# Kernel optimization log

Hardware: AMD Instinct MI355X
Metric: run time of the kernel (lower is better)

Reference implementation:

```python
import jax, jax.numpy as jnp
import numpy as np

EPS = 1e-5

def _sage_conv(x, src, dst, Wl, bl, Wr, num_nodes):
    # PyG SAGEConv (mean aggr): out = lin_l(mean_{j->i} x_j) + lin_r(x_i)
    msg = x[src]                                              # [E, F]
    s = jax.ops.segment_sum(msg, dst, num_segments=num_nodes) # [N, F]
    deg = jax.ops.segment_sum(jnp.ones(src.shape, x.dtype), dst, num_segments=num_nodes)
    mean = s / jnp.maximum(deg, 1.0)[:, None]
    return mean @ Wl + bl + x @ Wr

def _bn(x, gamma, beta):
    # BatchNorm1d in training mode: biased batch statistics
    m = x.mean(axis=0)
    v = x.var(axis=0)
    return (x - m) * jax.lax.rsqrt(v + EPS) * gamma + beta

def setup_inputs() -> dict:
    key = jax.random.key(0)
    ks = jax.random.split(key, 16)
    N, F, H, H1, H2 = 50000, 100, 128, 128, 64
    E = 800000
    def xav(k, fan_in, fan_out):
        lim = float(np.sqrt(6.0 / (fan_in + fan_out)))
        return jax.random.uniform(k, (fan_in, fan_out), jnp.float32, -lim, lim)
    return {
        "x": jax.random.normal(ks[0], (N, F), jnp.float32),
        "edge_index": jax.random.randint(ks[1], (2, E), 0, N, jnp.int32),
        "Wl1": xav(ks[2], F, H), "bl1": jnp.zeros((H,), jnp.float32), "Wr1": xav(ks[3], F, H),
        "Wl2": xav(ks[4], H, H), "bl2": jnp.zeros((H,), jnp.float32), "Wr2": xav(ks[5], H, H),
        "W1": xav(ks[6], H, H1), "b1": jnp.zeros((H1,), jnp.float32),
        "g1": jnp.ones((H1,), jnp.float32), "be1": jnp.zeros((H1,), jnp.float32),
        "W2": xav(ks[7], H1, H2), "b2": jnp.zeros((H2,), jnp.float32),
        "g2": jnp.ones((H2,), jnp.float32), "be2": jnp.zeros((H2,), jnp.float32),
        "W3": xav(ks[8], H2, 1), "b3": jnp.zeros((1,), jnp.float32),
    }

def reference(x, edge_index, Wl1, bl1, Wr1, Wl2, bl2, Wr2,
              W1, b1, g1, be1, W2, b2, g2, be2, W3, b3):
    N = x.shape[0]
    src, dst = edge_index[0], edge_index[1]
    h1 = jax.nn.relu(_sage_conv(x, src, dst, Wl1, bl1, Wr1, N))   # [N, H]
    h2 = jax.nn.relu(_sage_conv(h1, src, dst, Wl2, bl2, Wr2, N))  # [N, H]
    z = jax.nn.relu(_bn(h2 @ W1 + b1, g1, be1))                   # [N, H1]
    z = jax.nn.relu(_bn(z @ W2 + b2, g2, be2))                    # [N, H2]
    out = (z @ W3 + b3).squeeze(-1)                               # [N]
    return out, h1, h2
```

## Files before the change

kernel.cpp:

```cpp
#include <hip/hip_runtime.h>

#define BN_EPS 1e-5f

typedef short s8v __attribute__((ext_vector_type(8)));
typedef float f4v __attribute__((ext_vector_type(4)));
typedef unsigned short u4v __attribute__((ext_vector_type(4)));

__device__ __forceinline__ unsigned short f2bf(float f) {
  union { float f; unsigned u; } v; v.f = f;
  unsigned r = v.u + 0x7FFF + ((v.u >> 16) & 1);
  return (unsigned short)(r >> 16);
}
__device__ __forceinline__ float bf2f(unsigned short u) {
  union { unsigned u; float f; } v; v.u = ((unsigned)u) << 16; return v.f;
}

__global__ __launch_bounds__(256) void deg_kernel(const int* __restrict__ dst,
                                                  int* __restrict__ deg, int E) {
  int e = blockIdx.x * 256 + threadIdx.x;
  if (e < E) atomicAdd(&deg[dst[e]], 1);
}

__global__ __launch_bounds__(256) void scan_partial_kernel(const int* __restrict__ deg,
    int* __restrict__ partials, int N) {
  __shared__ int sh[256];
  int t = threadIdx.x;
  int base = blockIdx.x * 1024 + t * 4;
  int s = 0;
#pragma unroll
  for (int i = 0; i < 4; ++i) {
    int idx = base + i;
    if (idx < N) s += deg[idx];
  }
  sh[t] = s;
  __syncthreads();
  for (int d = 128; d > 0; d >>= 1) {
    if (t < d) sh[t] += sh[t + d];
    __syncthreads();
  }
  if (t == 0) partials[blockIdx.x] = sh[0];
}

__global__ __launch_bounds__(256) void scan_offsets_kernel(const int* __restrict__ partials,
    int* __restrict__ blk_off, int G) {
  __shared__ int sh[256];
  int t = threadIdx.x;
  sh[t] = (t < G) ? partials[t] : 0;
  __syncthreads();
  for (int d = 1; d < 256; d <<= 1) {
    int v = (t >= d) ? sh[t - d] : 0;
    __syncthreads();
    sh[t] += v;
    __syncthreads();
  }
  if (t < G) blk_off[t] = (t == 0) ? 0 : sh[t - 1];
}

__global__ __launch_bounds__(256) void scan_scatter_kernel(const int* __restrict__ deg,
    const int* __restrict__ blk_off, int* __restrict__ row_start,
    int* __restrict__ gcursor, int N) {
  __shared__ int sh[256];
  int t = threadIdx.x;
  int base = blockIdx.x * 1024 + t * 4;
  int v[4];
#pragma unroll
  for (int i = 0; i < 4; ++i) v[i] = (base + i < N) ? deg[base + i] : 0;
  sh[t] = v[0] + v[1] + v[2] + v[3];
  __syncthreads();
  for (int d = 1; d < 256; d <<= 1) {
    int u = (t >= d) ? sh[t - d] : 0;
    __syncthreads();
    sh[t] += u;
    __syncthreads();
  }
  int off = blk_off[blockIdx.x] + ((t == 0) ? 0 : sh[t - 1]);
#pragma unroll
  for (int i = 0; i < 4; ++i) {
    int idx = base + i;
    if (idx < N) {
      row_start[idx] = off;
      if ((idx & 127) == 0) gcursor[idx >> 7] = off;
      off += v[i];
    }
  }
}

#define CHUNK 8192
#define NBMAX 512
__global__ __launch_bounds__(256) void csr_bucket_kernel(
    const int* __restrict__ src, const int* __restrict__ dst,
    int* __restrict__ gcursor, unsigned* __restrict__ pairs, int E) {
  __shared__ int h[NBMAX];
  __shared__ int off[NBMAX];
  __shared__ int cnt2[NBMAX];
  __shared__ int gadj[NBMAX];
  __shared__ unsigned pbuf[CHUNK];
  __shared__ unsigned short bidx[CHUNK];
  int t = threadIdx.x;
  int base = blockIdx.x * CHUNK;
  int cnt = min(CHUNK, E - base);
  for (int i = t; i < NBMAX; i += 256) { h[i] = 0; cnt2[i] = 0; }
  __syncthreads();
  for (int i = t; i < cnt; i += 256) atomicAdd(&h[dst[base + i] >> 7], 1);
  __syncthreads();
  off[t] = h[t]; off[t + 256] = h[t + 256];
  __syncthreads();
  for (int d = 1; d < 512; d <<= 1) {
    int v0 = (t >= d) ? off[t - d] : 0;
    int v1 = off[t + 256 - d];
    __syncthreads();
    off[t] += v0; off[t + 256] += v1;
    __syncthreads();
  }
  int e0 = off[t] - h[t];
  int e1 = off[t + 256] - h[t + 256];
  __syncthreads();
  off[t] = e0; off[t + 256] = e1;
  __syncthreads();
  for (int i = t; i < NBMAX; i += 256) {
    int c = h[i];
    if (c > 0) gadj[i] = atomicAdd(&gcursor[i], c) - off[i];
  }
  __syncthreads();
  for (int i = t; i < cnt; i += 256) {
    int s = src[base + i];
    int d = dst[base + i];
    int b = d >> 7;
    int p = off[b] + atomicAdd(&cnt2[b], 1);
    pbuf[p] = (unsigned)s | ((unsigned)d << 16);
    bidx[p] = (unsigned short)b;
  }
  __syncthreads();
  for (int i = t; i < cnt; i += 256)
    pairs[gadj[bidx[i]] + i] = pbuf[i];
}

__global__ __launch_bounds__(256) void csr_fill_kernel(
    const unsigned* __restrict__ pairs, const int* __restrict__ row_start,
    int* __restrict__ eidx, int N, int E) {
  __shared__ int cur[128];
  int b = blockIdx.x;
  int node0 = b << 7;
  int t = threadIdx.x;
  if (t < 128) {
    int node = node0 + t;
    cur[t] = (node < N) ? row_start[node] : 0;
  }
  __syncthreads();
  int pbeg = row_start[node0];
  int pend = (node0 + 128 < N) ? row_start[node0 + 128] : E;
  for (int i = pbeg + t; i < pend; i += 256) {
    unsigned p = pairs[i];
    int pos = atomicAdd(&cur[(int)(p >> 16) - node0], 1);
    eidx[pos] = (int)(p & 0xFFFFu);
  }
}

__global__ __launch_bounds__(256) void prep_kernel(
    const float* __restrict__ x, unsigned short* __restrict__ xb,
    const float* __restrict__ Wl1, const float* __restrict__ Wr1,
    const float* __restrict__ Wl2, const float* __restrict__ Wr2,
    const float* __restrict__ W1, const float* __restrict__ W2,
    unsigned short* __restrict__ Wl1t, unsigned short* __restrict__ Wr1t,
    unsigned short* __restrict__ Wl2t, unsigned short* __restrict__ Wr2t,
    unsigned short* __restrict__ W1t, unsigned short* __restrict__ W2t,
    int N, int xblocks) {
  int blk = blockIdx.x;
  if (blk < xblocks) {
    int t = blk * 256 + threadIdx.x;
    if (t < N * 128) {
      int col = t & 127;
      int n = t >> 7;
      xb[t] = (col < 100) ? f2bf(x[n * 100 + col]) : (unsigned short)0;
    }
    return;
  }
  int w = blk - xblocks;
  const float* W; unsigned short* Wt; int K, C, base;
  if (w < 64)       { W = Wl1; Wt = Wl1t; K = 100; C = 128; base = 0;   }
  else if (w < 128) { W = Wr1; Wt = Wr1t; K = 100; C = 128; base = 64;  }
  else if (w < 192) { W = Wl2; Wt = Wl2t; K = 128; C = 128; base = 128; }
  else if (w < 256) { W = Wr2; Wt = Wr2t; K = 128; C = 128; base = 192; }
  else if (w < 320) { W = W1;  Wt = W1t;  K = 128; C = 128; base = 256; }
  else              { W = W2;  Wt = W2t;  K = 128; C = 64;  base = 320; }
  int t = (w - base) * 256 + threadIdx.x;
  if (t >= C * 128) return;
  int c = t >> 7;
  int k = t & 127;
  Wt[t] = (k < K) ? f2bf(W[k * C + c]) : (unsigned short)0;
}

__global__ __launch_bounds__(256) void gather_kernel(
    const unsigned short* __restrict__ feat, const int* __restrict__ eidx,
    const int* __restrict__ row_start, const int* __restrict__ deg,
    unsigned short* __restrict__ mean_out, int N) {
  int wave = threadIdx.x >> 6;
  int lane = threadIdx.x & 63;
  int node = blockIdx.x * 4 + wave;
  if (node >= N) return;
  int beg = row_start[node];
  int d = deg[node];
  float a0 = 0.0f, a1 = 0.0f;
  for (int i0 = 0; i0 < d; i0 += 64) {
    int cnt = min(64, d - i0);
    int my = (lane < cnt) ? eidx[beg + i0 + lane] : 0;
    int j = 0;
    for (; j + 7 < cnt; j += 8) {
      int s0 = __shfl(my, j + 0);
      int s1 = __shfl(my, j + 1);
      int s2 = __shfl(my, j + 2);
      int s3 = __shfl(my, j + 3);
      int s4 = __shfl(my, j + 4);
      int s5 = __shfl(my, j + 5);
      int s6 = __shfl(my, j + 6);
      int s7 = __shfl(my, j + 7);
      unsigned v0 = ((const unsigned*)(feat + (size_t)s0 * 128))[lane];
      unsigned v1 = ((const unsigned*)(feat + (size_t)s1 * 128))[lane];
      unsigned v2 = ((const unsigned*)(feat + (size_t)s2 * 128))[lane];
      unsigned v3 = ((const unsigned*)(feat + (size_t)s3 * 128))[lane];
      unsigned v4 = ((const unsigned*)(feat + (size_t)s4 * 128))[lane];
      unsigned v5 = ((const unsigned*)(feat + (size_t)s5 * 128))[lane];
      unsigned v6 = ((const unsigned*)(feat + (size_t)s6 * 128))[lane];
      unsigned v7 = ((const unsigned*)(feat + (size_t)s7 * 128))[lane];
      a0 += bf2f((unsigned short)v0) + bf2f((unsigned short)v1)
          + bf2f((unsigned short)v2) + bf2f((unsigned short)v3)
          + bf2f((unsigned short)v4) + bf2f((unsigned short)v5)
          + bf2f((unsigned short)v6) + bf2f((unsigned short)v7);
      a1 += bf2f((unsigned short)(v0 >> 16)) + bf2f((unsigned short)(v1 >> 16))
          + bf2f((unsigned short)(v2 >> 16)) + bf2f((unsigned short)(v3 >> 16))
          + bf2f((unsigned short)(v4 >> 16)) + bf2f((unsigned short)(v5 >> 16))
          + bf2f((unsigned short)(v6 >> 16)) + bf2f((unsigned short)(v7 >> 16));
    }
    for (; j < cnt; ++j) {
      int s0 = __shfl(my, j);
      unsigned v0 = ((const unsigned*)(feat + (size_t)s0 * 128))[lane];
      a0 += bf2f((unsigned short)v0);
      a1 += bf2f((unsigned short)(v0 >> 16));
    }
  }
  float inv = 1.0f / fmaxf((float)d, 1.0f);
  unsigned o = (unsigned)f2bf(a0 * inv) | ((unsigned)f2bf(a1 * inv) << 16);
  ((unsigned*)(mean_out + (size_t)node * 128))[lane] = o;
}

__global__ __launch_bounds__(128) void bn_prep_kernel(const float* __restrict__ sum,
    const float* __restrict__ sq, const float* __restrict__ g,
    const float* __restrict__ be, float* __restrict__ bnp, int N) {
  int c = threadIdx.x;
  float S = 0.0f, SS = 0.0f;
#pragma unroll
  for (int k = 0; k < 8; ++k) { S += sum[k * 128 + c]; SS += sq[k * 128 + c]; }
  float invN = 1.0f / (float)N;
  float mn = S * invN;
  float var = SS * invN - mn * mn;
  float sc = g[c] * rsqrtf(var + BN_EPS);
  bnp[2 * c] = sc;
  bnp[2 * c + 1] = be[c] - mn * sc;
}

template<int COLS, bool DUAL, bool RELU, bool F32OUT, bool BF16OUT, bool STATS, bool BNIN>
__global__ __launch_bounds__(256, 4) void mfma_gemm_kernel(
    const unsigned short* __restrict__ A1, const unsigned short* __restrict__ W1t,
    const unsigned short* __restrict__ A2, const unsigned short* __restrict__ W2t,
    const float* __restrict__ bias, const float* __restrict__ bnp,
    float* __restrict__ outF, unsigned short* __restrict__ outB,
    float* __restrict__ sum, float* __restrict__ sq, int N) {
  constexpr int CTW = COLS / 64;
  constexpr int CH = COLS / 4;
  constexpr int RS = COLS + 4;
  constexpr int NA = DUAL ? 2 : 1;
  constexpr int OUT_OFF = 8192 * NA;
  constexpr int BNL_OFF = OUT_OFF + 32 * RS * 4;
  constexpr int SMEM_SZ = BNL_OFF + (BNIN ? 1024 : 0);
  __shared__ char smem[SMEM_SZ];
  float* outl = (float*)(smem + OUT_OFF);
  float* reds = (float*)smem;
  float* redq = (float*)(smem + 4096);
  float* bnl  = (float*)(smem + BNL_OFF);
  int t = threadIdx.x;
  int wave = t >> 6;
  int lane = t & 63;
  int quad = lane >> 4;
  int m = lane & 15;
  int blk = blockIdx.x * 32;
  int col0 = wave * (16 * CTW);

  if (BNIN) bnl[t] = bnp[t];

  s8v B1r[4][CTW], B2r[4][CTW];
  {
    int c0 = wave * 2, c1 = c0 + 1;
    const char* g1 = (const char*)A1 + (size_t)blk * 256;
    s8v va = *(const s8v*)(g1 + c0 * 1024 + lane * 16);
    s8v vb = *(const s8v*)(g1 + c1 * 1024 + lane * 16);
    s8v vc, vd;
    if (DUAL) {
      const char* g2 = (const char*)A2 + (size_t)blk * 256;
      vc = *(const s8v*)(g2 + c0 * 1024 + lane * 16);
      vd = *(const s8v*)(g2 + c1 * 1024 + lane * 16);
    }
#pragma unroll
    for (int kk = 0; kk < 4; ++kk)
#pragma unroll
      for (int ct = 0; ct < CTW; ++ct) {
        size_t wr = (size_t)(col0 + ct * 16 + m) * 128 + kk * 32 + quad * 8;
        B1r[kk][ct] = *(const s8v*)(W1t + wr);
        if (DUAL) B2r[kk][ct] = *(const s8v*)(W2t + wr);
      }
    int r0 = c0 * 4 + (lane >> 4);
    int r1 = r0 + 4;
    int cb = (lane & 15) << 4;
    *(s8v*)(smem + r0 * 256 + (cb ^ ((r0 & 7) << 4))) = va;
    *(s8v*)(smem + r1 * 256 + (cb ^ ((r1 & 7) << 4))) = vb;
    if (DUAL) {
      *(s8v*)(smem + 8192 + r0 * 256 + (cb ^ ((r0 & 7) << 4))) = vc;
      *(s8v*)(smem + 8192 + r1 * 256 + (cb ^ ((r1 & 7) << 4))) = vd;
    }
  }
  __syncthreads();

  f4v acc[2][CTW];
#pragma unroll
  for (int rf = 0; rf < 2; ++rf)
#pragma unroll
    for (int ct = 0; ct < CTW; ++ct) acc[rf][ct] = (f4v){0.f, 0.f, 0.f, 0.f};
#pragma unroll
  for (int kk = 0; kk < 4; ++kk) {
    int cb2 = kk * 64 + quad * 16;
    s8v a1[2], a2[2];
#pragma unroll
    for (int rf = 0; rf < 2; ++rf) {
      int rr = rf * 16 + m;
      int sw = rr * 256 + (cb2 ^ ((rr & 7) << 4));
      a1[rf] = *(const s8v*)(smem + sw);
      if (DUAL) a2[rf] = *(const s8v*)(smem + 8192 + sw);
    }
    if (BNIN) {
      float sc[8], sh[8];
#pragma unroll
      for (int i = 0; i < 8; ++i) {
        int c = kk * 32 + quad * 8 + i;
        sc[i] = bnl[2 * c]; sh[i] = bnl[2 * c + 1];
      }
#pragma unroll
      for (int rf = 0; rf < 2; ++rf) {
        s8v raw = a1[rf];
        s8v a;
#pragma unroll
        for (int i = 0; i < 8; ++i) {
          float v = bf2f((unsigned short)raw[i]);
          v = fmaxf(v * sc[i] + sh[i], 0.0f);
          a[i] = (short)f2bf(v);
        }
        a1[rf] = a;
      }
    }
#pragma unroll
    for (int ct = 0; ct < CTW; ++ct)
#pragma unroll
      for (int rf = 0; rf < 2; ++rf) {
        acc[rf][ct] = __builtin_amdgcn_mfma_f32_16x16x32_bf16(a1[rf], B1r[kk][ct], acc[rf][ct], 0, 0, 0);
        if (DUAL)
          acc[rf][ct] = __builtin_amdgcn_mfma_f32_16x16x32_bf16(a2[rf], B2r[kk][ct], acc[rf][ct], 0, 0, 0);
      }
  }

#pragma unroll
  for (int ct = 0; ct < CTW; ++ct) {
    int col = col0 + ct * 16 + m;
    float b = bias[col];
#pragma unroll
    for (int rf = 0; rf < 2; ++rf)
#pragma unroll
      for (int r = 0; r < 4; ++r) {
        float v = acc[rf][ct][r] + b;
        if (RELU) v = fmaxf(v, 0.0f);
        outl[(rf * 16 + quad * 4 + r) * RS + col] = v;
      }
  }
  __syncthreads();
  float s4[4] = {0.f, 0.f, 0.f, 0.f}, q4[4] = {0.f, 0.f, 0.f, 0.f};
  for (int idx = t; idx < 32 * CH; idx += 256) {
    int row = idx / CH;
    int c4 = idx % CH;
    int gr = blk + row;
    if (gr < N) {
      f4v v = *(const f4v*)&outl[row * RS + c4 * 4];
      if (F32OUT) *(f4v*)(outF + (size_t)gr * COLS + c4 * 4) = v;
      if (BF16OUT) {
        u4v o;
#pragma unroll
        for (int j = 0; j < 4; ++j) o[j] = f2bf(v[j]);
        *(u4v*)(outB + (size_t)gr * COLS + c4 * 4) = o;
      }
      if (STATS) {
#pragma unroll
        for (int j = 0; j < 4; ++j) { s4[j] += v[j]; q4[j] += v[j] * v[j]; }
      }
    }
  }
  if (STATS) {
    __syncthreads();
#pragma unroll
    for (int j = 0; j < 4; ++j) { reds[t * 4 + j] = s4[j]; redq[t * 4 + j] = q4[j]; }
    __syncthreads();
    if (t < COLS) {
      int c4 = t >> 2, j = t & 3;
      float S = 0.0f, SS = 0.0f;
#pragma unroll
      for (int g = 0; g < 256 / CH; ++g) {
        S  += reds[(g * CH + c4) * 4 + j];
        SS += redq[(g * CH + c4) * 4 + j];
      }
      int slot = (blockIdx.x & 7) * COLS + t;
      atomicAdd(&sum[slot], S);
      atomicAdd(&sq[slot], SS);
    }
  }
}

__global__ __launch_bounds__(256, 4) void sage_mlp_kernel(
    const unsigned short* __restrict__ A1,
    const unsigned short* __restrict__ Wlt,
    const unsigned short* __restrict__ A2,
    const unsigned short* __restrict__ Wrt,
    const float* __restrict__ bl,
    const unsigned short* __restrict__ W1t, const float* __restrict__ b1,
    float* __restrict__ h2out, unsigned short* __restrict__ y1b,
    float* __restrict__ sum, float* __restrict__ sq, int N) {
  constexpr int RS = 132;
  constexpr int OUT_OFF = 16384;
  __shared__ char smem[OUT_OFF + 32 * RS * 4];
  float* outl = (float*)(smem + OUT_OFF);
  float* reds = (float*)smem;
  float* redq = (float*)(smem + 4096);
  int t = threadIdx.x;
  int wave = t >> 6, lane = t & 63;
  int quad = lane >> 4, m = lane & 15;
  int blk = blockIdx.x * 32;
  int col0 = wave * 32;

  s8v BLr[4][2], BRr[4][2];
  {
    int c0 = wave * 2, c1 = c0 + 1;
    const char* g1 = (const char*)A1 + (size_t)blk * 256;
    const char* g2 = (const char*)A2 + (size_t)blk * 256;
    s8v va = *(const s8v*)(g1 + c0 * 1024 + lane * 16);
    s8v vb = *(const s8v*)(g1 + c1 * 1024 + lane * 16);
    s8v vc = *(const s8v*)(g2 + c0 * 1024 + lane * 16);
    s8v vd = *(const s8v*)(g2 + c1 * 1024 + lane * 16);
#pragma unroll
    for (int kk = 0; kk < 4; ++kk)
#pragma unroll
      for (int ct = 0; ct < 2; ++ct) {
        size_t wr = (size_t)(col0 + ct * 16 + m) * 128 + kk * 32 + quad * 8;
        BLr[kk][ct] = *(const s8v*)(Wlt + wr);
        BRr[kk][ct] = *(const s8v*)(Wrt + wr);
      }
    int r0 = c0 * 4 + (lane >> 4);
    int r1 = r0 + 4;
    int cb = (lane & 15) << 4;
    *(s8v*)(smem + r0 * 256 + (cb ^ ((r0 & 7) << 4))) = va;
    *(s8v*)(smem + r1 * 256 + (cb ^ ((r1 & 7) << 4))) = vb;
    *(s8v*)(smem + 8192 + r0 * 256 + (cb ^ ((r0 & 7) << 4))) = vc;
    *(s8v*)(smem + 8192 + r1 * 256 + (cb ^ ((r1 & 7) << 4))) = vd;
  }
  __syncthreads();

  f4v acc[2][2];
#pragma unroll
  for (int rf = 0; rf < 2; ++rf)
#pragma unroll
    for (int ct = 0; ct < 2; ++ct) acc[rf][ct] = (f4v){0.f, 0.f, 0.f, 0.f};
#pragma unroll
  for (int kk = 0; kk < 4; ++kk) {
    int cb2 = kk * 64 + quad * 16;
    s8v a1[2], a2[2];
#pragma unroll
    for (int rf = 0; rf < 2; ++rf) {
      int rr = rf * 16 + m;
      int sw = rr * 256 + (cb2 ^ ((rr & 7) << 4));
      a1[rf] = *(const s8v*)(smem + sw);
      a2[rf] = *(const s8v*)(smem + 8192 + sw);
    }
#pragma unroll
    for (int ct = 0; ct < 2; ++ct)
#pragma unroll
      for (int rf = 0; rf < 2; ++rf) {
        acc[rf][ct] = __builtin_amdgcn_mfma_f32_16x16x32_bf16(a1[rf], BLr[kk][ct], acc[rf][ct], 0, 0, 0);
        acc[rf][ct] = __builtin_amdgcn_mfma_f32_16x16x32_bf16(a2[rf], BRr[kk][ct], acc[rf][ct], 0, 0, 0);
      }
  }

  s8v bw[4][2];
#pragma unroll
  for (int kk = 0; kk < 4; ++kk)
#pragma unroll
    for (int ct = 0; ct < 2; ++ct)
      bw[kk][ct] = *(const s8v*)(W1t + (size_t)(col0 + ct * 16 + m) * 128 + kk * 32 + quad * 8);

#pragma unroll
  for (int ct = 0; ct < 2; ++ct) {
    int col = col0 + ct * 16 + m;
    float b = bl[col];
#pragma unroll
    for (int rf = 0; rf < 2; ++rf)
#pragma unroll
      for (int r = 0; r < 4; ++r)
        outl[(rf * 16 + quad * 4 + r) * RS + col] = fmaxf(acc[rf][ct][r] + b, 0.0f);
  }
  __syncthreads();

  for (int idx = t; idx < 32 * 32; idx += 256) {
    int row = idx >> 5;
    int c4 = idx & 31;
    int gr = blk + row;
    if (gr < N)
      *(f4v*)(h2out + (size_t)gr * 128 + c4 * 4) = *(const f4v*)&outl[row * RS + c4 * 4];
  }

  s8v af[2][4];
#pragma unroll
  for (int rf = 0; rf < 2; ++rf)
#pragma unroll
    for (int kk = 0; kk < 4; ++kk) {
      int k0 = kk * 32 + quad * 8;
      f4v x0 = *(const f4v*)&outl[(rf * 16 + m) * RS + k0];
      f4v x1 = *(const f4v*)&outl[(rf * 16 + m) * RS + k0 + 4];
      s8v a;
#pragma unroll
      for (int i = 0; i < 4; ++i) { a[i] = (short)f2bf(x0[i]); a[4 + i] = (short)f2bf(x1[i]); }
      af[rf][kk] = a;
    }

  f4v acc2[2][2];
#pragma unroll
  for (int rf = 0; rf < 2; ++rf)
#pragma unroll
    for (int ct = 0; ct < 2; ++ct) acc2[rf][ct] = (f4v){0.f, 0.f, 0.f, 0.f};
#pragma unroll
  for (int kk = 0; kk < 4; ++kk)
#pragma unroll
    for (int ct = 0; ct < 2; ++ct)
#pragma unroll
      for (int rf = 0; rf < 2; ++rf)
        acc2[rf][ct] = __builtin_amdgcn_mfma_f32_16x16x32_bf16(af[rf][kk], bw[kk][ct], acc2[rf][ct], 0, 0, 0);
  __syncthreads();
#pragma unroll
  for (int ct = 0; ct < 2; ++ct) {
    int col = col0 + ct * 16 + m;
    float b = b1[col];
#pragma unroll
    for (int rf = 0; rf < 2; ++rf)
#pragma unroll
      for (int r = 0; r < 4; ++r)
        outl[(rf * 16 + quad * 4 + r) * RS + col] = acc2[rf][ct][r] + b;
  }
  __syncthreads();

  float s4[4] = {0.f, 0.f, 0.f, 0.f}, q4[4] = {0.f, 0.f, 0.f, 0.f};
  for (int idx = t; idx < 32 * 32; idx += 256) {
    int row = idx >> 5;
    int c4 = idx & 31;
    int gr = blk + row;
    if (gr < N) {
      f4v v = *(const f4v*)&outl[row * RS + c4 * 4];
      u4v o;
#pragma unroll
      for (int j = 0; j < 4; ++j) o[j] = f2bf(v[j]);
      *(u4v*)(y1b + (size_t)gr * 128 + c4 * 4) = o;
#pragma unroll
      for (int j = 0; j < 4; ++j) { s4[j] += v[j]; q4[j] += v[j] * v[j]; }
    }
  }
#pragma unroll
  for (int j = 0; j < 4; ++j) { reds[t * 4 + j] = s4[j]; redq[t * 4 + j] = q4[j]; }
  __syncthreads();
  if (t < 128) {
    int c4 = t >> 2, j = t & 3;
    float S = 0.0f, SS = 0.0f;
#pragma unroll
    for (int g = 0; g < 8; ++g) {
      S  += reds[(g * 32 + c4) * 4 + j];
      SS += redq[(g * 32 + c4) * 4 + j];
    }
    int slot = (blockIdx.x & 7) * 128 + t;
    atomicAdd(&sum[slot], S);
    atomicAdd(&sq[slot], SS);
  }
}

__global__ __launch_bounds__(256) void bn_head_kernel(const float* __restrict__ y2,
    const float* __restrict__ sum, const float* __restrict__ sumsq,
    const float* __restrict__ g, const float* __restrict__ be,
    const float* __restrict__ W3, const float* __restrict__ b3,
    float* __restrict__ out, int N) {
  int wave = threadIdx.x >> 6;
  int lane = threadIdx.x & 63;
  int row = blockIdx.x * 4 + wave;
  if (row >= N) return;
  float S = 0.0f, SS = 0.0f;
#pragma unroll
  for (int k = 0; k < 8; ++k) { S += sum[k * 64 + lane]; SS += sumsq[k * 64 + lane]; }
  float invN = 1.0f / (float)N;
  float m = S * invN;
  float var = SS * invN - m * m;
  float val = (y2[(size_t)row * 64 + lane] - m) * rsqrtf(var + BN_EPS) * g[lane] + be[lane];
  val = fmaxf(val, 0.0f) * W3[lane];
#pragma unroll
  for (int off = 32; off > 0; off >>= 1) val += __shfl_down(val, off);
  if (lane == 0) out[row] = val + b3[0];
}

extern "C" void kernel_launch(void* const* d_in, const int* in_sizes, int n_in,
                              void* d_out, int out_size, void* d_ws, size_t ws_size,
                              hipStream_t stream) {
  const int F = 100, H = 128;
  const int N = in_sizes[0] / F;
  const int E = in_sizes[1] / 2;

  const float* x   = (const float*)d_in[0];
  const int* edge  = (const int*)d_in[1];
  const int* src   = edge;
  const int* dst   = edge + E;
  const float* Wl1 = (const float*)d_in[2];
  const float* bl1 = (const float*)d_in[3];
  const float* Wr1 = (const float*)d_in[4];
  const float* Wl2 = (const float*)d_in[5];
  const float* bl2 = (const float*)d_in[6];
  const float* Wr2 = (const float*)d_in[7];
  const float* W1  = (const float*)d_in[8];
  const float* b1  = (const float*)d_in[9];
  const float* g1  = (const float*)d_in[10];
  const float* be1 = (const float*)d_in[11];
  const float* W2  = (const float*)d_in[12];
  const float* b2  = (const float*)d_in[13];
  const float* g2  = (const float*)d_in[14];
  const float* be2 = (const float*)d_in[15];
  const float* W3  = (const float*)d_in[16];
  const float* b3  = (const float*)d_in[17];

  float* out0 = (float*)d_out;
  float* h1   = out0 + N;
  float* h2   = h1 + (size_t)N * H;

  const int SCAN_G = (N + 1023) / 1024;
  const int NB = (N + 127) / 128;

  char* wsp = (char*)d_ws;
  int* deg       = (int*)wsp;               wsp += (size_t)N * sizeof(int);
  int* row_start = (int*)wsp;               wsp += (size_t)N * sizeof(int);
  int* eidx      = (int*)wsp;               wsp += (size_t)E * sizeof(int);
  unsigned* pairs = (unsigned*)wsp;         wsp += (size_t)E * sizeof(unsigned);
  int* gcursor   = (int*)wsp;               wsp += 512 * sizeof(int);
  int* partials  = (int*)wsp;               wsp += 256 * sizeof(int);
  int* blk_off   = (int*)wsp;               wsp += 256 * sizeof(int);
  float* sum1    = (float*)wsp;             wsp += 8 * 128 * sizeof(float);
  float* sq1     = (float*)wsp;             wsp += 8 * 128 * sizeof(float);
  float* sum2    = (float*)wsp;             wsp += 8 * 64 * sizeof(float);
  float* sq2     = (float*)wsp;             wsp += 8 * 64 * sizeof(float);
  float* bnp     = (float*)wsp;             wsp += 256 * sizeof(float);
  float* bufA    = (float*)wsp;             wsp += (size_t)N * 128 * sizeof(float);
  unsigned short* bfX = (unsigned short*)wsp; wsp += (size_t)N * 128 * 2;
  unsigned short* bfM = (unsigned short*)wsp; wsp += (size_t)N * 128 * 2;
  unsigned short* bfH = (unsigned short*)wsp; wsp += (size_t)N * 128 * 2;
  unsigned short* Wl1t = (unsigned short*)wsp; wsp += 128 * 128 * 2;
  unsigned short* Wr1t = (unsigned short*)wsp; wsp += 128 * 128 * 2;
  unsigned short* Wl2t = (unsigned short*)wsp; wsp += 128 * 128 * 2;
  unsigned short* Wr2t = (unsigned short*)wsp; wsp += 128 * 128 * 2;
  unsigned short* W1t  = (unsigned short*)wsp; wsp += 128 * 128 * 2;
  unsigned short* W2t  = (unsigned short*)wsp; wsp += 64 * 128 * 2;

  unsigned short* y1b = (unsigned short*)bufA;
  float* y2 = (float*)((char*)bufA + (size_t)N * 128 * 2);

  hipMemsetAsync(deg, 0, (size_t)N * sizeof(int), stream);
  hipMemsetAsync(sum1, 0, (8 * 128 + 8 * 128 + 8 * 64 + 8 * 64) * sizeof(float), stream);

  deg_kernel<<<(E + 255) / 256, 256, 0, stream>>>(dst, deg, E);
  scan_partial_kernel<<<SCAN_G, 256, 0, stream>>>(deg, partials, N);
  scan_offsets_kernel<<<1, 256, 0, stream>>>(partials, blk_off, SCAN_G);
  scan_scatter_kernel<<<SCAN_G, 256, 0, stream>>>(deg, blk_off, row_start, gcursor, N);
  csr_bucket_kernel<<<(E + CHUNK - 1) / CHUNK, 256, 0, stream>>>(src, dst, gcursor, pairs, E);
  csr_fill_kernel<<<NB, 256, 0, stream>>>(pairs, row_start, eidx, N, E);

  int xblocks = ((size_t)N * 128 + 255) / 256;
  prep_kernel<<<xblocks + 352, 256, 0, stream>>>(x, bfX,
      Wl1, Wr1, Wl2, Wr2, W1, W2, Wl1t, Wr1t, Wl2t, Wr2t, W1t, W2t, N, xblocks);

  int gemm_grid = (N + 31) / 32;

  gather_kernel<<<(N + 3) / 4, 256, 0, stream>>>(bfX, eidx, row_start, deg, bfM, N);
  mfma_gemm_kernel<128, true, true, true, true, false, false><<<gemm_grid, 256, 0, stream>>>(
      bfM, Wl1t, bfX, Wr1t, bl1, nullptr, h1, bfH, nullptr, nullptr, N);

  gather_kernel<<<(N + 3) / 4, 256, 0, stream>>>(bfH, eidx, row_start, deg, bfM, N);
  sage_mlp_kernel<<<gemm_grid, 256, 0, stream>>>(
      bfM, Wl2t, bfH, Wr2t, bl2, W1t, b1, h2, y1b, sum1, sq1, N);

  bn_prep_kernel<<<1, 128, 0, stream>>>(sum1, sq1, g1, be1, bnp, N);

  mfma_gemm_kernel<64, false, false, true, false, true, true><<<gemm_grid, 256, 0, stream>>>(
      y1b, W2t, nullptr, nullptr, b2, bnp, y2, nullptr, sum2, sq2, N);

  bn_head_kernel<<<(N + 3) / 4, 256, 0, stream>>>(
      y2, sum2, sq2, g2, be2, W3, b3, out0, N);
}
```

Baseline: 323.5 us.

## Merge small setup kernels and fold BN prep into GEMM to cut launches

Folds the degree-count atomics into the prep kernel and replaces the three-kernel prefix scan with a single 1024-thread block scan. The BN statistics finalisation is now computed redundantly in each block of the second MLP GEMM, so bn_prep_kernel is gone, and the two memsets are merged into one by placing the BN accumulators next to the degree array. It also halves the CSR bucket chunk size and raises the occupancy hint for the non-dual GEMM. The intent is to remove several kernel launches and serialization points, at the cost of a serial single-block scan and repeated per-block BN math.

```diff
diff --git a/kernel.cpp b/kernel.cpp
--- a/kernel.cpp
+++ b/kernel.cpp
@@ -15,77 +15,78 @@
   union { unsigned u; float f; } v; v.u = ((unsigned)u) << 16; return v.f;
 }
 
-__global__ __launch_bounds__(256) void deg_kernel(const int* __restrict__ dst,
-                                                  int* __restrict__ deg, int E) {
-  int e = blockIdx.x * 256 + threadIdx.x;
-  if (e < E) atomicAdd(&deg[dst[e]], 1);
-}
-
-__global__ __launch_bounds__(256) void scan_partial_kernel(const int* __restrict__ deg,
-    int* __restrict__ partials, int N) {
-  __shared__ int sh[256];
+__global__ __launch_bounds__(256) void prep_kernel(
+    const int* __restrict__ dst, int* __restrict__ deg, int E, int degB,
+    const float* __restrict__ x, unsigned short* __restrict__ xb,
+    const float* __restrict__ Wl1, const float* __restrict__ Wr1,
+    const float* __restrict__ Wl2, const float* __restrict__ Wr2,
+    const float* __restrict__ W1, const float* __restrict__ W2,
+    unsigned short* __restrict__ Wl1t, unsigned short* __restrict__ Wr1t,
+    unsigned short* __restrict__ Wl2t, unsigned short* __restrict__ Wr2t,
+    unsigned short* __restrict__ W1t, unsigned short* __restrict__ W2t,
+    int N, int xblocks) {
+  int blk = blockIdx.x;
+  if (blk < degB) {
+    int e = blk * 256 + threadIdx.x;
+    if (e < E) atomicAdd(&deg[dst[e]], 1);
+    return;
+  }
+  blk -= degB;
+  if (blk < xblocks) {
+    int t = blk * 256 + threadIdx.x;
+    if (t < N * 128) {
+      int col = t & 127;
+      int n = t >> 7;
+      xb[t] = (col < 100) ? f2bf(x[n * 100 + col]) : (unsigned short)0;
+    }
+    return;
+  }
+  int w = blk - xblocks;
+  const float* W; unsigned short* Wt; int K, C, base;
+  if (w < 64)       { W = Wl1; Wt = Wl1t; K = 100; C = 128; base = 0;   }
+  else if (w < 128) { W = Wr1; Wt = Wr1t; K = 100; C = 128; base = 64;  }
+  else if (w < 192) { W = Wl2; Wt = Wl2t; K = 128; C = 128; base = 128; }
+  else if (w < 256) { W = Wr2; Wt = Wr2t; K = 128; C = 128; base = 192; }
+  else if (w < 320) { W = W1;  Wt = W1t;  K = 128; C = 128; base = 256; }
+  else              { W = W2;  Wt = W2t;  K = 128; C = 64;  base = 320; }
+  int t = (w - base) * 256 + threadIdx.x;
+  if (t >= C * 128) return;
+  int c = t >> 7;
+  int k = t & 127;
+  Wt[t] = (k < K) ? f2bf(W[k * C + c]) : (unsigned short)0;
+}
+
+__global__ __launch_bounds__(1024) void scan_all_kernel(const int* __restrict__ deg,
+    int* __restrict__ row_start, int* __restrict__ gcursor, int N) {
+  __shared__ int ws[1024];
   int t = threadIdx.x;
-  int base = blockIdx.x * 1024 + t * 4;
+  int PER = (N + 1023) >> 10;
+  int base = t * PER;
   int s = 0;
-#pragma unroll
-  for (int i = 0; i < 4; ++i) {
+  for (int i = 0; i < PER; ++i) {
     int idx = base + i;
     if (idx < N) s += deg[idx];
   }
-  sh[t] = s;
-  __syncthreads();
-  for (int d = 128; d > 0; d >>= 1) {
-    if (t < d) sh[t] += sh[t + d];
+  ws[t] = s;
+  __syncthreads();
+  for (int d = 1; d < 1024; d <<= 1) {
+    int v = (t >= d) ? ws[t - d] : 0;
     __syncthreads();
-  }
-  if (t == 0) partials[blockIdx.x] = sh[0];
-}
-
-__global__ __launch_bounds__(256) void scan_offsets_kernel(const int* __restrict__ partials,
-    int* __restrict__ blk_off, int G) {
-  __shared__ int sh[256];
-  int t = threadIdx.x;
-  sh[t] = (t < G) ? partials[t] : 0;
-  __syncthreads();
-  for (int d = 1; d < 256; d <<= 1) {
-    int v = (t >= d) ? sh[t - d] : 0;
+    ws[t] += v;
     __syncthreads();
-    sh[t] += v;
-    __syncthreads();
-  }
-  if (t < G) blk_off[t] = (t == 0) ? 0 : sh[t - 1];
-}
-
-__global__ __launch_bounds__(256) void scan_scatter_kernel(const int* __restrict__ deg,
-    const int* __restrict__ blk_off, int* __restrict__ row_start,
-    int* __restrict__ gcursor, int N) {
-  __shared__ int sh[256];
-  int t = threadIdx.x;
-  int base = blockIdx.x * 1024 + t * 4;
-  int v[4];
-#pragma unroll
-  for (int i = 0; i < 4; ++i) v[i] = (base + i < N) ? deg[base + i] : 0;
-  sh[t] = v[0] + v[1] + v[2] + v[3];
-  __syncthreads();
-  for (int d = 1; d < 256; d <<= 1) {
-    int u = (t >= d) ? sh[t - d] : 0;
-    __syncthreads();
-    sh[t] += u;
-    __syncthreads();
-  }
-  int off = blk_off[blockIdx.x] + ((t == 0) ? 0 : sh[t - 1]);
-#pragma unroll
-  for (int i = 0; i < 4; ++i) {
+  }
+  int off = (t == 0) ? 0 : ws[t - 1];
+  for (int i = 0; i < PER; ++i) {
     int idx = base + i;
     if (idx < N) {
       row_start[idx] = off;
       if ((idx & 127) == 0) gcursor[idx >> 7] = off;
-      off += v[i];
-    }
-  }
-}
-
-#define CHUNK 8192
+      off += deg[idx];
+    }
+  }
+}
+
+#define CHUNK 4096
 #define NBMAX 512
 __global__ __launch_bounds__(256) void csr_bucket_kernel(
     const int* __restrict__ src, const int* __restrict__ dst,
@@ -154,40 +155,6 @@
     int pos = atomicAdd(&cur[(int)(p >> 16) - node0], 1);
     eidx[pos] = (int)(p & 0xFFFFu);
   }
-}
-
-__global__ __launch_bounds__(256) void prep_kernel(
-    const float* __restrict__ x, unsigned short* __restrict__ xb,
-    const float* __restrict__ Wl1, const float* __restrict__ Wr1,
-    const float* __restrict__ Wl2, const float* __restrict__ Wr2,
-    const float* __restrict__ W1, const float* __restrict__ W2,
-    unsigned short* __restrict__ Wl1t, unsigned short* __restrict__ Wr1t,
-    unsigned short* __restrict__ Wl2t, unsigned short* __restrict__ Wr2t,
-    unsigned short* __restrict__ W1t, unsigned short* __restrict__ W2t,
-    int N, int xblocks) {
-  int blk = blockIdx.x;
-  if (blk < xblocks) {
-    int t = blk * 256 + threadIdx.x;
-    if (t < N * 128) {
-      int col = t & 127;
-      int n = t >> 7;
-      xb[t] = (col < 100) ? f2bf(x[n * 100 + col]) : (unsigned short)0;
-    }
-    return;
-  }
-  int w = blk - xblocks;
-  const float* W; unsigned short* Wt; int K, C, base;
-  if (w < 64)       { W = Wl1; Wt = Wl1t; K = 100; C = 128; base = 0;   }
-  else if (w < 128) { W = Wr1; Wt = Wr1t; K = 100; C = 128; base = 64;  }
-  else if (w < 192) { W = Wl2; Wt = Wl2t; K = 128; C = 128; base = 128; }
-  else if (w < 256) { W = Wr2; Wt = Wr2t; K = 128; C = 128; base = 192; }
-  else if (w < 320) { W = W1;  Wt = W1t;  K = 128; C = 128; base = 256; }
-  else              { W = W2;  Wt = W2t;  K = 128; C = 64;  base = 320; }
-  int t = (w - base) * 256 + threadIdx.x;
-  if (t >= C * 128) return;
-  int c = t >> 7;
-  int k = t & 127;
-  Wt[t] = (k < K) ? f2bf(W[k * C + c]) : (unsigned short)0;
 }
 
 __global__ __launch_bounds__(256) void gather_kernel(
@@ -243,26 +210,13 @@
   ((unsigned*)(mean_out + (size_t)node * 128))[lane] = o;
 }
 
-__global__ __launch_bounds__(128) void bn_prep_kernel(const float* __restrict__ sum,
-    const float* __restrict__ sq, const float* __restrict__ g,
-    const float* __restrict__ be, float* __restrict__ bnp, int N) {
-  int c = threadIdx.x;
-  float S = 0.0f, SS = 0.0f;
-#pragma unroll
-  for (int k = 0; k < 8; ++k) { S += sum[k * 128 + c]; SS += sq[k * 128 + c]; }
-  float invN = 1.0f / (float)N;
-  float mn = S * invN;
-  float var = SS * invN - mn * mn;
-  float sc = g[c] * rsqrtf(var + BN_EPS);
-  bnp[2 * c] = sc;
-  bnp[2 * c + 1] = be[c] - mn * sc;
-}
-
 template<int COLS, bool DUAL, bool RELU, bool F32OUT, bool BF16OUT, bool STATS, bool BNIN>
-__global__ __launch_bounds__(256, 4) void mfma_gemm_kernel(
+__global__ __launch_bounds__(256, DUAL ? 4 : 5) void mfma_gemm_kernel(
     const unsigned short* __restrict__ A1, const unsigned short* __restrict__ W1t,
     const unsigned short* __restrict__ A2, const unsigned short* __restrict__ W2t,
-    const float* __restrict__ bias, const float* __restrict__ bnp,
+    const float* __restrict__ bias,
+    const float* __restrict__ bsum, const float* __restrict__ bsq,
+    const float* __restrict__ bg, const float* __restrict__ bbe,
     float* __restrict__ outF, unsigned short* __restrict__ outB,
     float* __restrict__ sum, float* __restrict__ sq, int N) {
   constexpr int CTW = COLS / 64;
@@ -285,7 +239,17 @@
   int blk = blockIdx.x * 32;
   int col0 = wave * (16 * CTW);
 
-  if (BNIN) bnl[t] = bnp[t];
+  if (BNIN && t < 128) {
+    float S = 0.0f, SS = 0.0f;
+#pragma unroll
+    for (int k = 0; k < 8; ++k) { S += bsum[k * 128 + t]; SS += bsq[k * 128 + t]; }
+    float invN = 1.0f / (float)N;
+    float mn = S * invN;
+    float var = SS * invN - mn * mn;
+    float sc = bg[t] * rsqrtf(var + BN_EPS);
+    bnl[2 * t] = sc;
+    bnl[2 * t + 1] = bbe[t] - mn * sc;
+  }
 
   s8v B1r[4][CTW], B2r[4][CTW];
   {
@@ -644,22 +608,18 @@
   float* h1   = out0 + N;
   float* h2   = h1 + (size_t)N * H;
 
-  const int SCAN_G = (N + 1023) / 1024;
   const int NB = (N + 127) / 128;
 
   char* wsp = (char*)d_ws;
   int* deg       = (int*)wsp;               wsp += (size_t)N * sizeof(int);
+  float* sum1    = (float*)wsp;             wsp += 8 * 128 * sizeof(float);
+  float* sq1     = (float*)wsp;             wsp += 8 * 128 * sizeof(float);
+  float* sum2    = (float*)wsp;             wsp += 8 * 64 * sizeof(float);
+  float* sq2     = (float*)wsp;             wsp += 8 * 64 * sizeof(float);
   int* row_start = (int*)wsp;               wsp += (size_t)N * sizeof(int);
   int* eidx      = (int*)wsp;               wsp += (size_t)E * sizeof(int);
   unsigned* pairs = (unsigned*)wsp;         wsp += (size_t)E * sizeof(unsigned);
   int* gcursor   = (int*)wsp;               wsp += 512 * sizeof(int);
-  int* partials  = (int*)wsp;               wsp += 256 * sizeof(int);
-  int* blk_off   = (int*)wsp;               wsp += 256 * sizeof(int);
-  float* sum1    = (float*)wsp;             wsp += 8 * 128 * sizeof(float);
-  float* sq1     = (float*)wsp;             wsp += 8 * 128 * sizeof(float);
-  float* sum2    = (float*)wsp;             wsp += 8 * 64 * sizeof(float);
-  float* sq2     = (float*)wsp;             wsp += 8 * 64 * sizeof(float);
-  float* bnp     = (float*)wsp;             wsp += 256 * sizeof(float);
   float* bufA    = (float*)wsp;             wsp += (size_t)N * 128 * sizeof(float);
   unsigned short* bfX = (unsigned short*)wsp; wsp += (size_t)N * 128 * 2;
   unsigned short* bfM = (unsigned short*)wsp; wsp += (size_t)N * 128 * 2;
@@ -674,34 +634,29 @@
   unsigned short* y1b = (unsigned short*)bufA;
   float* y2 = (float*)((char*)bufA + (size_t)N * 128 * 2);
 
-  hipMemsetAsync(deg, 0, (size_t)N * sizeof(int), stream);
-  hipMemsetAsync(sum1, 0, (8 * 128 + 8 * 128 + 8 * 64 + 8 * 64) * sizeof(float), stream);
-
-  deg_kernel<<<(E + 255) / 256, 256, 0, stream>>>(dst, deg, E);
-  scan_partial_kernel<<<SCAN_G, 256, 0, stream>>>(deg, partials, N);
-  scan_offsets_kernel<<<1, 256, 0, stream>>>(partials, blk_off, SCAN_G);
-  scan_scatter_kernel<<<SCAN_G, 256, 0, stream>>>(deg, blk_off, row_start, gcursor, N);
+  hipMemsetAsync(deg, 0, (size_t)N * sizeof(int) + (8 * 128 * 2 + 8 * 64 * 2) * sizeof(float), stream);
+
+  int degB = (E + 255) / 256;
+  int xblocks = ((size_t)N * 128 + 255) / 256;
+  prep_kernel<<<degB + xblocks + 352, 256, 0, stream>>>(dst, deg, E, degB, x, bfX,
+      Wl1, Wr1, Wl2, Wr2, W1, W2, Wl1t, Wr1t, Wl2t, Wr2t, W1t, W2t, N, xblocks);
+
+  scan_all_kernel<<<1, 1024, 0, stream>>>(deg, row_start, gcursor, N);
   csr_bucket_kernel<<<(E + CHUNK - 1) / CHUNK, 256, 0, stream>>>(src, dst, gcursor, pairs, E);
   csr_fill_kernel<<<NB, 256, 0, stream>>>(pairs, row_start, eidx, N, E);
 
-  int xblocks = ((size_t)N * 128 + 255) / 256;
-  prep_kernel<<<xblocks + 352, 256, 0, stream>>>(x, bfX,
-      Wl1, Wr1, Wl2, Wr2, W1, W2, Wl1t, Wr1t, Wl2t, Wr2t, W1t, W2t, N, xblocks);
-
   int gemm_grid = (N + 31) / 32;
 
   gather_kernel<<<(N + 3) / 4, 256, 0, stream>>>(bfX, eidx, row_start, deg, bfM, N);
   mfma_gemm_kernel<128, true, true, true, true, false, false><<<gemm_grid, 256, 0, stream>>>(
-      bfM, Wl1t, bfX, Wr1t, bl1, nullptr, h1, bfH, nullptr, nullptr, N);
+      bfM, Wl1t, bfX, Wr1t, bl1, nullptr, nullptr, nullptr, nullptr, h1, bfH, nullptr, nullptr, N);
 
   gather_kernel<<<(N + 3) / 4, 256, 0, stream>>>(bfH, eidx, row_start, deg, bfM, N);
   sage_mlp_kernel<<<gemm_grid, 256, 0, stream>>>(
       bfM, Wl2t, bfH, Wr2t, bl2, W1t, b1, h2, y1b, sum1, sq1, N);
 
-  bn_prep_kernel<<<1, 128, 0, stream>>>(sum1, sq1, g1, be1, bnp, N);
-
   mfma_gemm_kernel<64, false, false, true, false, true, true><<<gemm_grid, 256, 0, stream>>>(
-      y1b, W2t, nullptr, nullptr, b2, bnp, y2, nullptr, sum2, sq2, N);
+      y1b, W2t, nullptr, nullptr, b2, sum1, sq1, g1, be1, y2, nullptr, sum2, sq2, N);
 
   bn_head_kernel<<<(N + 3) / 4, 256, 0, stream>>>(
       y2, sum2, sq2, g2, be2, W3, b3, out0, N);
```

New measurement: 396.9 us. +22.7%, slower.
